# Kernel optimization log

Measured on AMD Instinct MI355X. Metric: run time of the kernel, lower is better.

## Reference

```python
import jax, jax.numpy as jnp
import numpy as np

B, T, C, H = 128, 256, 384, 6
D = C // H  # head dim = 64


def setup_inputs() -> dict:
    key = jax.random.key(0)
    k1, k2, k3, k4, k5 = jax.random.split(key, 5)
    s = 0.02
    return {
        "x": jax.random.normal(k1, (B, T, C), dtype=jnp.float32),
        "W_qkv": jax.random.normal(k2, (C, 3 * C), dtype=jnp.float32) * s,
        "b_qkv": jax.random.normal(k3, (3 * C,), dtype=jnp.float32) * s,
        "W_proj": jax.random.normal(k4, (C, C), dtype=jnp.float32) * s,
        "b_proj": jax.random.normal(k5, (C,), dtype=jnp.float32) * s,
    }


def reference(x, W_qkv, b_qkv, W_proj, b_proj):
    Bv, Tv, Cv = x.shape
    # fused QKV projection, then split
    qkv = x @ W_qkv + b_qkv                      # [B,T,3C]
    q, k, v = jnp.split(qkv, 3, axis=-1)
    # [B,T,C] -> [B,H,T,D]
    q = q.reshape(Bv, Tv, H, D).transpose(0, 2, 1, 3)
    k = k.reshape(Bv, Tv, H, D).transpose(0, 2, 1, 3)
    v = v.reshape(Bv, Tv, H, D).transpose(0, 2, 1, 3)
    # causal masked scores, scaled by head_dim**-0.5
    scores = jnp.einsum("bhqd,bhkd->bhqk", q, k) * (D ** -0.5)
    causal = jnp.tril(jnp.ones((Tv, Tv), dtype=bool))
    scores = jnp.where(causal, scores, -jnp.inf)
    wt = jax.nn.softmax(scores, axis=-1)
    # dropout layers are identity in eval mode
    out = jnp.einsum("bhqk,bhkd->bhqd", wt, v)   # [B,H,T,D]
    out = out.transpose(0, 2, 1, 3).reshape(Bv, Tv, Cv)
    return out @ W_proj + b_proj
```

## Files before the change

### kernel.cpp

```cpp
#include <hip/hip_runtime.h>

typedef unsigned short u16;
typedef unsigned int u32;
typedef __attribute__((ext_vector_type(4))) float f32x4;
typedef __attribute__((ext_vector_type(8))) __bf16 bf16x8;
typedef __attribute__((ext_vector_type(2))) __bf16 bf16x2;

#define NEGINF (-1e30f)
#define QSCALE 0.18033688011112042f

__device__ __forceinline__ u16 f32_to_bf16(float f) {
  union { float f; unsigned int u; } v;
  v.f = f;
  unsigned int u = v.u;
  u += 0x7fffu + ((u >> 16) & 1u);
  return (u16)(u >> 16);
}

__device__ __forceinline__ u32 pk_bf16(float a, float b) {
  bf16x2 t;
  t.x = (__bf16)a;
  t.y = (__bf16)b;
  return __builtin_bit_cast(u32, t);
}

__device__ __forceinline__ f32x4 mfma_bf16(bf16x8 a, bf16x8 b, f32x4 c) {
  return __builtin_amdgcn_mfma_f32_16x16x32_bf16(a, b, c, 0, 0, 0);
}

#define GLOAD_LDS16(g, l) __builtin_amdgcn_global_load_lds( \
    (const __attribute__((address_space(1))) unsigned int*)(g), \
    (__attribute__((address_space(3))) unsigned int*)(l), 16, 0, 0)

__global__ void k_cvt4(const float4* __restrict__ in, u16* __restrict__ out, int nq) {
  int i = blockIdx.x * blockDim.x + threadIdx.x;
  if (i >= nq) return;
  float4 v = in[i];
  uint2 o;
  o.x = (unsigned int)f32_to_bf16(v.x) | ((unsigned int)f32_to_bf16(v.y) << 16);
  o.y = (unsigned int)f32_to_bf16(v.z) | ((unsigned int)f32_to_bf16(v.w) << 16);
  *(uint2*)(out + (size_t)i * 4) = o;
}

__global__ void k_tcvt(const float* __restrict__ in, u16* __restrict__ out, int K, int N) {
  int idx = blockIdx.x * blockDim.x + threadIdx.x;
  if (idx >= K * N) return;
  int k = idx / N, n = idx - k * N;
  out[(size_t)n * K + k] = f32_to_bf16(in[idx]);
}

template <bool SW>
__device__ __forceinline__ void gemm256x64(
    const u16* __restrict__ A, const u16* __restrict__ Bt,
    int mBase, int nBase, u16* lsA, u16* lsB,
    f32x4 acc[4][2], int lane, int wv, int wm, int wn) {
  const int l15 = lane & 15;
  size_t aoff[4];
  u32 aldso[4];
#pragma unroll
  for (int jj = 0; jj < 4; ++jj) {
    int c = wv * 256 + jj * 64 + lane;
    int row = c >> 3;
    int kc = (c & 7) ^ (row & 7);
    aoff[jj] = (size_t)(mBase + row) * 384 + kc * 8;
    aldso[jj] = (u32)(wv * 256 + jj * 64) * 8;
  }
  int cb = wv * 64 + lane;
  int brow = cb >> 3;
  size_t boff = (size_t)(nBase + brow) * 384 + (size_t)(((cb & 7) ^ (brow & 7)) * 8);
  u32 bldso = (u32)(wv * 64) * 8;

#define STAGE_T(kt, buf) do { \
  _Pragma("unroll") \
  for (int jj = 0; jj < 4; ++jj) \
    GLOAD_LDS16(A + aoff[jj] + (kt), lsA + (buf) * 16384 + aldso[jj]); \
  GLOAD_LDS16(Bt + boff + (kt), lsB + (buf) * 4096 + bldso); \
  } while (0)

  STAGE_T(0, 0);
#pragma unroll
  for (int t = 0; t < 6; ++t) {
    const int cur = t & 1;
    if (t < 5) {
      STAGE_T((t + 1) * 64, cur ^ 1);
      asm volatile("s_waitcnt vmcnt(5)" ::: "memory");
    } else {
      asm volatile("s_waitcnt vmcnt(0)" ::: "memory");
    }
    __builtin_amdgcn_s_barrier();
    const char* bA = (const char*)(lsA + cur * 16384);
    const char* bB = (const char*)(lsB + cur * 4096);
#pragma unroll
    for (int ks = 0; ks < 2; ++ks) {
      bf16x8 af[4], bfr[2];
#pragma unroll
      for (int i = 0; i < 4; ++i) {
        int row = wm * 64 + i * 16 + l15;
        af[i] = *(const bf16x8*)(bA + row * 128 + (((ks * 4 + (lane >> 4)) ^ (row & 7)) << 4));
      }
#pragma unroll
      for (int j = 0; j < 2; ++j) {
        int row = wn * 32 + j * 16 + l15;
        bfr[j] = *(const bf16x8*)(bB + row * 128 + (((ks * 4 + (lane >> 4)) ^ (row & 7)) << 4));
      }
#pragma unroll
      for (int i = 0; i < 4; ++i)
#pragma unroll
        for (int j = 0; j < 2; ++j)
          acc[i][j] = SW ? mfma_bf16(bfr[j], af[i], acc[i][j])
                         : mfma_bf16(af[i], bfr[j], acc[i][j]);
    }
    __builtin_amdgcn_s_barrier();
  }
#undef STAGE_T
}

__global__ __launch_bounds__(512, 4) void k_qkv(
    const u16* __restrict__ A, const u16* __restrict__ Bt,
    const float* __restrict__ bias,
    u16* __restrict__ Qb, u16* __restrict__ Kb, u16* __restrict__ Vtb) {
  __shared__ __align__(16) u16 lsA[2 * 16384];
  __shared__ __align__(16) u16 lsB[2 * 4096];
  const int tid = threadIdx.x, lane = tid & 63, wv = tid >> 6;
  const int l15 = lane & 15, g = lane >> 4;
  const int wm = wv >> 1, wn = wv & 1;
  const int bid = (int)blockIdx.x;
  const int wgid = (bid & 7) * 288 + (bid >> 3);
  const int mtile = wgid / 18, ntile = wgid % 18;
  const int mBase = mtile * 256, nBase = ntile * 64;
  const int part = ntile / 6;
  const int hh = ntile % 6;
  char* ot = (char*)lsA;

  f32x4 acc[4][2] = {};
  if (part == 2) {
    gemm256x64<false>(A, Bt, mBase, nBase, lsA, lsB, acc, lane, wv, wm, wn);
#pragma unroll
    for (int j = 0; j < 2; ++j) {
      int drow = wn * 32 + j * 16 + l15;
      float bv = bias[nBase + drow];
#pragma unroll
      for (int i = 0; i < 4; ++i) {
        int t0 = wm * 64 + i * 16 + g * 4;
        uint2 w;
        w.x = pk_bf16(acc[i][j][0] + bv, acc[i][j][1] + bv);
        w.y = pk_bf16(acc[i][j][2] + bv, acc[i][j][3] + bv);
        int byte = (drow * 512 + t0 * 2) ^ ((drow & 7) << 4);
        *(uint2*)(ot + byte) = w;
      }
    }
    asm volatile("s_waitcnt lgkmcnt(0)" ::: "memory");
    __builtin_amdgcn_s_barrier();
    size_t obase = (size_t)(mtile * 6 + hh) * (64 * 256);
#pragma unroll
    for (int p = 0; p < 4; ++p) {
      int idx = p * 512 + tid;
      int row = idx >> 5, c = idx & 31;
      uint4 v = *(const uint4*)(ot + row * 512 + (((c ^ (row & 7)) << 4)));
      *(uint4*)(Vtb + obase + (size_t)row * 256 + c * 8) = v;
    }
  } else {
    gemm256x64<true>(A, Bt, mBase, nBase, lsA, lsB, acc, lane, wv, wm, wn);
    const float scale = (part == 0) ? QSCALE : 1.0f;
    u16* dst = (part == 0) ? Qb : Kb;
#pragma unroll
    for (int j = 0; j < 2; ++j) {
      int dbase = wn * 32 + j * 16 + g * 4;
      float4 bv4 = *(const float4*)(bias + nBase + dbase);
#pragma unroll
      for (int i = 0; i < 4; ++i) {
        int trow = wm * 64 + i * 16 + l15;
        uint2 w;
        w.x = pk_bf16((acc[i][j][0] + bv4.x) * scale, (acc[i][j][1] + bv4.y) * scale);
        w.y = pk_bf16((acc[i][j][2] + bv4.z) * scale, (acc[i][j][3] + bv4.w) * scale);
        int byte = (trow * 128 + dbase * 2) ^ ((trow & 7) << 4);
        *(uint2*)(ot + byte) = w;
      }
    }
    asm volatile("s_waitcnt lgkmcnt(0)" ::: "memory");
    __builtin_amdgcn_s_barrier();
    size_t obase = (size_t)(mtile * 6 + hh) * (256 * 64);
#pragma unroll
    for (int p = 0; p < 4; ++p) {
      int idx = p * 512 + tid;
      int row = idx >> 3, c = idx & 7;
      uint4 v = *(const uint4*)(ot + row * 128 + (((c ^ (row & 7)) << 4)));
      *(uint4*)(dst + obase + (size_t)row * 64 + c * 8) = v;
    }
  }
}

__global__ __launch_bounds__(64, 3) void k_attn(
    const u16* __restrict__ Qb, const u16* __restrict__ Kb,
    const u16* __restrict__ Vtb, u16* __restrict__ Ob) {
  __shared__ __align__(16) u16 lsP[32 * 64];
  const int lane = threadIdx.x;
  const int l15 = lane & 15, g = lane >> 4;
  const int s = 7 - (int)blockIdx.y;
  const int bh = blockIdx.x;
  const int b = bh / 6, h = bh % 6;
  const u16* Qh = Qb + (size_t)bh * (256 * 64);
  const u16* Kh = Kb + (size_t)bh * (256 * 64);
  const u16* Vh = Vtb + (size_t)bh * (64 * 256);
  const int ktiles = (s >> 1) + 1;
  char* pbuf = (char*)lsP;

  bf16x8 qf[2][2];
#pragma unroll
  for (int ks = 0; ks < 2; ++ks)
#pragma unroll
    for (int iq = 0; iq < 2; ++iq)
      qf[ks][iq] = *(const bf16x8*)(Qh + (size_t)(s * 32 + iq * 16 + l15) * 64 + ks * 32 + g * 8);

  f32x4 o[4][2] = {};
  float rl[2] = {0.f, 0.f};

#pragma unroll 1
  for (int kt = 0; kt < ktiles; ++kt) {
    bf16x8 kf[2][4];
#pragma unroll
    for (int ks = 0; ks < 2; ++ks)
#pragma unroll
      for (int jk = 0; jk < 4; ++jk)
        kf[ks][jk] = *(const bf16x8*)(Kh + (size_t)(kt * 64 + jk * 16 + l15) * 64 + ks * 32 + g * 8);

    f32x4 st[4][2] = {};
    __builtin_amdgcn_s_setprio(1);
#pragma unroll
    for (int ks = 0; ks < 2; ++ks)
#pragma unroll
      for (int jk = 0; jk < 4; ++jk)
#pragma unroll
        for (int iq = 0; iq < 2; ++iq)
          st[jk][iq] = mfma_bf16(kf[ks][jk], qf[ks][iq], st[jk][iq]);
    __builtin_amdgcn_s_setprio(0);

    bf16x8 vf[2][4];
#pragma unroll
    for (int ks = 0; ks < 2; ++ks)
#pragma unroll
      for (int jd = 0; jd < 4; ++jd)
        vf[ks][jd] = *(const bf16x8*)(Vh + (size_t)(jd * 16 + l15) * 256 + kt * 64 + ks * 32 + g * 8);

    if (kt == ktiles - 1) {
#pragma unroll
      for (int jk = 0; jk < 4; ++jk)
#pragma unroll
        for (int iq = 0; iq < 2; ++iq)
#pragma unroll
          for (int r = 0; r < 4; ++r)
            if (kt * 64 + jk * 16 + g * 4 + r > s * 32 + iq * 16 + l15)
              st[jk][iq][r] = NEGINF;
    }

    float rs[2] = {0.f, 0.f};
#pragma unroll
    for (int jk = 0; jk < 4; ++jk)
#pragma unroll
      for (int iq = 0; iq < 2; ++iq) {
        float p0 = __builtin_amdgcn_exp2f(st[jk][iq][0]);
        float p1 = __builtin_amdgcn_exp2f(st[jk][iq][1]);
        float p2 = __builtin_amdgcn_exp2f(st[jk][iq][2]);
        float p3 = __builtin_amdgcn_exp2f(st[jk][iq][3]);
        rs[iq] += (p0 + p1) + (p2 + p3);
        int q = iq * 16 + l15;
        int byte = (q * 128 + (jk * 16 + g * 4) * 2) ^ ((q & 7) << 4);
        uint2 w;
        w.x = pk_bf16(p0, p1);
        w.y = pk_bf16(p2, p3);
        *(uint2*)(pbuf + byte) = w;
      }
#pragma unroll
    for (int iq = 0; iq < 2; ++iq) {
      float v = rs[iq];
      v += __shfl_xor(v, 16);
      v += __shfl_xor(v, 32);
      rl[iq] += v;
    }

#pragma unroll
    for (int ks = 0; ks < 2; ++ks) {
      bf16x8 pf[2];
#pragma unroll
      for (int iq = 0; iq < 2; ++iq) {
        int q = iq * 16 + l15;
        pf[iq] = *(const bf16x8*)(pbuf + ((q * 128 + ks * 64 + g * 16) ^ ((q & 7) << 4)));
      }
      __builtin_amdgcn_s_setprio(1);
#pragma unroll
      for (int jd = 0; jd < 4; ++jd)
#pragma unroll
        for (int iq = 0; iq < 2; ++iq)
          o[jd][iq] = mfma_bf16(vf[ks][jd], pf[iq], o[jd][iq]);
      __builtin_amdgcn_s_setprio(0);
    }
  }

#pragma unroll
  for (int iq = 0; iq < 2; ++iq) {
    float inv = 1.0f / rl[iq];
    int q = iq * 16 + l15;
#pragma unroll
    for (int jd = 0; jd < 4; ++jd) {
      uint2 w;
      w.x = pk_bf16(o[jd][iq][0] * inv, o[jd][iq][1] * inv);
      w.y = pk_bf16(o[jd][iq][2] * inv, o[jd][iq][3] * inv);
      int byte = (q * 128 + jd * 32 + g * 8) ^ ((q & 7) << 4);
      *(uint2*)(pbuf + byte) = w;
    }
  }
  asm volatile("s_waitcnt lgkmcnt(0)" ::: "memory");
#pragma unroll
  for (int rep = 0; rep < 4; ++rep) {
    int row = rep * 8 + (lane >> 3);
    int c = lane & 7;
    uint4 v = *(const uint4*)(pbuf + row * 128 + ((c ^ (row & 7)) * 16));
    int t = s * 32 + row;
    *(uint4*)(Ob + ((size_t)(b * 256 + t)) * 384 + h * 64 + c * 8) = v;
  }
}

__device__ __forceinline__ void gemm128sq(
    const u16* __restrict__ A, const u16* __restrict__ Bt,
    int mBase, int nBase, u16* lsA, u16* lsB,
    f32x4 acc[4][4], int lane, int wv) {
  const int l15 = lane & 15, g = lane >> 4;
  const int wm = wv >> 1, wn = wv & 1;
  size_t aoff[4], boff[4];
  u32 ldso[4];
#pragma unroll
  for (int jj = 0; jj < 4; ++jj) {
    int c = jj * 256 + wv * 64 + lane;
    int row = c >> 3;
    int kc = (c & 7) ^ (row & 7);
    aoff[jj] = (size_t)(mBase + row) * 384 + kc * 8;
    boff[jj] = (size_t)(nBase + row) * 384 + kc * 8;
    ldso[jj] = (u32)c * 8;
  }
#pragma unroll 1
  for (int t = 0; t < 6; ++t) {
#pragma unroll
    for (int jj = 0; jj < 4; ++jj) {
      GLOAD_LDS16(A + aoff[jj] + t * 64, lsA + ldso[jj]);
      GLOAD_LDS16(Bt + boff[jj] + t * 64, lsB + ldso[jj]);
    }
    __syncthreads();
#pragma unroll
    for (int ks = 0; ks < 2; ++ks) {
      bf16x8 af[4], bfr[4];
#pragma unroll
      for (int i = 0; i < 4; ++i) {
        int row = wm * 64 + i * 16 + l15;
        af[i] = *(const bf16x8*)((const char*)lsA + row * 128 + (((ks * 4 + g) ^ (row & 7)) << 4));
      }
#pragma unroll
      for (int j = 0; j < 4; ++j) {
        int row = wn * 64 + j * 16 + l15;
        bfr[j] = *(const bf16x8*)((const char*)lsB + row * 128 + (((ks * 4 + g) ^ (row & 7)) << 4));
      }
      __builtin_amdgcn_s_setprio(1);
#pragma unroll
      for (int i = 0; i < 4; ++i)
#pragma unroll
        for (int j = 0; j < 4; ++j)
          acc[i][j] = mfma_bf16(af[i], bfr[j], acc[i][j]);
      __builtin_amdgcn_s_setprio(0);
    }
    __syncthreads();
  }
}

__global__ __launch_bounds__(256, 3) void k_proj(
    const u16* __restrict__ A, const u16* __restrict__ Bt,
    const float* __restrict__ bias, float* __restrict__ out) {
  __shared__ __align__(16) u16 lsA[8192];
  __shared__ __align__(16) u16 lsB[8192];
  const int tid = threadIdx.x, lane = tid & 63, wv = tid >> 6;
  const int l15 = lane & 15, g = lane >> 4;
  const int wm = wv >> 1, wn = wv & 1;
  const int bid = (int)blockIdx.x;
  const int wgid = (bid & 7) * 96 + (bid >> 3);
  const int mBase = (wgid / 3) * 128, nBase = (wgid % 3) * 128;
  f32x4 acc[4][4] = {};
  gemm128sq(A, Bt, mBase, nBase, lsA, lsB, acc, lane, wv);
#pragma unroll
  for (int j = 0; j < 4; ++j) {
    int col = nBase + wn * 64 + j * 16 + l15;
    float bv = bias[col];
#pragma unroll
    for (int i = 0; i < 4; ++i) {
      int m0 = mBase + wm * 64 + i * 16 + g * 4;
#pragma unroll
      for (int r = 0; r < 4; ++r)
        out[(size_t)(m0 + r) * 384 + col] = acc[i][j][r] + bv;
    }
  }
}

extern "C" void kernel_launch(void* const* d_in, const int* in_sizes, int n_in,
                              void* d_out, int out_size, void* d_ws, size_t ws_size,
                              hipStream_t stream) {
  const float* x     = (const float*)d_in[0];
  const float* Wqkv  = (const float*)d_in[1];
  const float* bqkv  = (const float*)d_in[2];
  const float* Wproj = (const float*)d_in[3];
  const float* bproj = (const float*)d_in[4];
  float* out = (float*)d_out;

  char* ws = (char*)d_ws;
  u16* xb     = (u16*)(ws);
  u16* wqkvb  = (u16*)(ws + 25165824);
  u16* wprojb = (u16*)(ws + 26050560);
  u16* Qb     = (u16*)(ws + 26345472);
  u16* Kb     = (u16*)(ws + 51511296);
  u16* Vtb    = (u16*)(ws + 76677120);
  u16* Ob     = (u16*)(ws + 101842944);

  k_cvt4<<<12288, 256, 0, stream>>>((const float4*)x, xb, 3145728);
  k_tcvt<<<1728, 256, 0, stream>>>(Wqkv, wqkvb, 384, 1152);
  k_tcvt<<<576, 256, 0, stream>>>(Wproj, wprojb, 384, 384);
  k_qkv<<<2304, 512, 0, stream>>>(xb, wqkvb, bqkv, Qb, Kb, Vtb);
  k_attn<<<dim3(768, 8), 64, 0, stream>>>(Qb, Kb, Vtb, Ob);
  k_proj<<<768, 256, 0, stream>>>(Ob, wprojb, bproj, out);
}
```

Measured before the change: 121.8 us.

## Merge conversion kernels and pack four attention q-tiles per block

Three fp32-to-bf16 conversion launches become a single launch that dispatches on block index. The attention kernel moves from 64-thread blocks, one per 32-row query tile, to 256-thread blocks with four independent waves. The waves pair q-tiles (7,6,1,0) and (5,4,3,2) so each block has equal causal work. This cuts launch overhead and block count and balances per-block work, at the cost of four LDS P buffers per block and changed occupancy bounds.

```diff
diff --git a/kernel.cpp b/kernel.cpp
--- a/kernel.cpp
+++ b/kernel.cpp
@@ -32,21 +32,30 @@
     (const __attribute__((address_space(1))) unsigned int*)(g), \
     (__attribute__((address_space(3))) unsigned int*)(l), 16, 0, 0)
 
-__global__ void k_cvt4(const float4* __restrict__ in, u16* __restrict__ out, int nq) {
-  int i = blockIdx.x * blockDim.x + threadIdx.x;
-  if (i >= nq) return;
-  float4 v = in[i];
-  uint2 o;
-  o.x = (unsigned int)f32_to_bf16(v.x) | ((unsigned int)f32_to_bf16(v.y) << 16);
-  o.y = (unsigned int)f32_to_bf16(v.z) | ((unsigned int)f32_to_bf16(v.w) << 16);
-  *(uint2*)(out + (size_t)i * 4) = o;
-}
-
-__global__ void k_tcvt(const float* __restrict__ in, u16* __restrict__ out, int K, int N) {
-  int idx = blockIdx.x * blockDim.x + threadIdx.x;
-  if (idx >= K * N) return;
-  int k = idx / N, n = idx - k * N;
-  out[(size_t)n * K + k] = f32_to_bf16(in[idx]);
+__global__ void k_cvt_all(const float4* __restrict__ x4, u16* __restrict__ xb,
+                          const float* __restrict__ Wqkv, u16* __restrict__ wqkvb,
+                          const float* __restrict__ Wproj, u16* __restrict__ wprojb) {
+  const int bidx = (int)blockIdx.x;
+  if (bidx < 12288) {
+    int i = bidx * 256 + threadIdx.x;
+    float4 v = x4[i];
+    uint2 o;
+    o.x = (unsigned int)f32_to_bf16(v.x) | ((unsigned int)f32_to_bf16(v.y) << 16);
+    o.y = (unsigned int)f32_to_bf16(v.z) | ((unsigned int)f32_to_bf16(v.w) << 16);
+    *(uint2*)(xb + (size_t)i * 4) = o;
+  } else if (bidx < 14016) {
+    int idx = (bidx - 12288) * 256 + threadIdx.x;
+    if (idx < 384 * 1152) {
+      int k = idx / 1152, n = idx - k * 1152;
+      wqkvb[(size_t)n * 384 + k] = f32_to_bf16(Wqkv[idx]);
+    }
+  } else {
+    int idx = (bidx - 14016) * 256 + threadIdx.x;
+    if (idx < 384 * 384) {
+      int k = idx / 384, n = idx - k * 384;
+      wprojb[(size_t)n * 384 + k] = f32_to_bf16(Wproj[idx]);
+    }
+  }
 }
 
 template <bool SW>
@@ -190,20 +199,20 @@
   }
 }
 
-__global__ __launch_bounds__(64, 3) void k_attn(
+__global__ __launch_bounds__(256, 4) void k_attn(
     const u16* __restrict__ Qb, const u16* __restrict__ Kb,
     const u16* __restrict__ Vtb, u16* __restrict__ Ob) {
-  __shared__ __align__(16) u16 lsP[32 * 64];
-  const int lane = threadIdx.x;
+  __shared__ __align__(16) u16 lsP[4][32 * 64];
+  const int lane = threadIdx.x & 63, wv = threadIdx.x >> 6;
   const int l15 = lane & 15, g = lane >> 4;
-  const int s = 7 - (int)blockIdx.y;
+  const int s = blockIdx.y ? (5 - wv) : ((wv < 2) ? 7 - wv : 3 - wv);
   const int bh = blockIdx.x;
   const int b = bh / 6, h = bh % 6;
   const u16* Qh = Qb + (size_t)bh * (256 * 64);
   const u16* Kh = Kb + (size_t)bh * (256 * 64);
   const u16* Vh = Vtb + (size_t)bh * (64 * 256);
   const int ktiles = (s >> 1) + 1;
-  char* pbuf = (char*)lsP;
+  char* pbuf = (char*)&lsP[wv][0];
 
   bf16x8 qf[2][2];
 #pragma unroll
@@ -416,10 +425,8 @@
   u16* Vtb    = (u16*)(ws + 76677120);
   u16* Ob     = (u16*)(ws + 101842944);
 
-  k_cvt4<<<12288, 256, 0, stream>>>((const float4*)x, xb, 3145728);
-  k_tcvt<<<1728, 256, 0, stream>>>(Wqkv, wqkvb, 384, 1152);
-  k_tcvt<<<576, 256, 0, stream>>>(Wproj, wprojb, 384, 384);
+  k_cvt_all<<<14592, 256, 0, stream>>>((const float4*)x, xb, Wqkv, wqkvb, Wproj, wprojb);
   k_qkv<<<2304, 512, 0, stream>>>(xb, wqkvb, bqkv, Qb, Kb, Vtb);
-  k_attn<<<dim3(768, 8), 64, 0, stream>>>(Qb, Kb, Vtb, Ob);
+  k_attn<<<dim3(768, 2), 256, 0, stream>>>(Qb, Kb, Vtb, Ob);
   k_proj<<<768, 256, 0, stream>>>(Ob, wprojb, bproj, out);
 }
```

Result: slower. 129.2 us (+6.1%).
